# Kernel tuning notes

Measured on AMD Instinct MI355X. Metric: run time of the kernel, lower is better.

Reference implementation:

```python
import jax, jax.numpy as jnp
import numpy as np
from jax.scipy.special import erf

B, N, D = 4, 4096, 2
MU, ALPHA, BETA, SIGMA = 1.0, 0.8, 2.0, 0.02


def setup_inputs() -> dict:
    key = jax.random.key(0)
    k1, k2 = jax.random.split(key)
    locations = jax.random.uniform(k1, (B, N, D), dtype=jnp.float32)  # events in unit box
    times = jnp.sort(jax.random.uniform(k2, (B, N), dtype=jnp.float32), axis=-1)  # sorted event times
    # ragged sequence lengths via mask
    lengths = jnp.array([N, N - 256, N - 512, N - 1024], dtype=jnp.int32)
    mask = jnp.arange(N)[None, :] < lengths[:, None]
    return {
        "locations": locations,
        "times": times,
        "mask": mask,
        "mu": jnp.float32(MU),
        "alpha": jnp.float32(ALPHA),
        "beta": jnp.float32(BETA),
        "sigma": jnp.float32(SIGMA),
        "spatial_low": jnp.zeros((D,), jnp.float32),
        "spatial_high": jnp.ones((D,), jnp.float32),
        "t_end": jnp.float32(1.0),
    }


def reference(locations, times, mask, mu, alpha, beta, sigma, spatial_low, spatial_high, t_end):
    """Hawkes log_prob: sum_i log lambda*(s_i, t_i | H_{t_i}) - Lambda(D x [0, T])."""
    d = locations.shape[-1]
    # --- intensity at each event given its (strictly earlier, masked) history ---
    dt = times[:, :, None] - times[:, None, :]            # [B,N,N] t_i - t_j
    valid = (dt > 0.0) & mask[:, None, :]                 # causal + observed history
    dt_safe = jnp.where(valid, dt, 0.0)
    diff = locations[:, :, None, :] - locations[:, None, :, :]  # [B,N,N,D]
    sqdist = jnp.sum(diff * diff, axis=-1)                # [B,N,N]
    two_sig2 = 2.0 * sigma * sigma
    # fused exp of temporal decay * spatial Gaussian exponent
    kern = jnp.where(valid, jnp.exp(-beta * dt_safe - sqdist / two_sig2), 0.0)
    norm = beta / (jnp.pi * two_sig2) ** (d / 2)          # beta * (2*pi*sigma^2)^(-d/2)
    lam = mu + alpha * norm * jnp.sum(kern, axis=-1)      # [B,N]
    log_lam = jnp.sum(jnp.where(mask, jnp.log(lam), 0.0), axis=-1)  # [B]
    # --- compensator with erf boundary correction ---
    s_sqrt2 = sigma * jnp.sqrt(jnp.float32(2.0))
    cdf = 0.5 * (erf((spatial_high - locations) / s_sqrt2)
                 - erf((spatial_low - locations) / s_sqrt2))        # [B,N,D]
    in_domain_mass = jnp.prod(cdf, axis=-1)               # [B,N]
    temporal_mass = 1.0 - jnp.exp(-beta * (t_end - times))  # [B,N]
    area = jnp.prod(spatial_high - spatial_low)
    comp = mu * area * t_end + alpha * jnp.sum(
        jnp.where(mask, temporal_mass * in_domain_mass, 0.0), axis=-1)  # [B]
    return log_lam - comp
```

## Files before the change

### kernel.cpp

```cpp
#include <hip/hip_runtime.h>
#include <math.h>

#define NB 4096
#define BB 4
#define TI 256
#define TJ 256

#if __has_builtin(__builtin_amdgcn_exp2f)
#define EXP2F __builtin_amdgcn_exp2f
#else
#define EXP2F exp2f
#endif

__global__ __launch_bounds__(TI) void hawkes_pair(
    const float* __restrict__ loc, const float* __restrict__ times,
    const int* __restrict__ mask,
    const float* __restrict__ beta_p, const float* __restrict__ sigma_p,
    float* __restrict__ S)
{
    const int it = blockIdx.x;
    const int s  = blockIdx.y;
    if (s > it) return;
    const int b   = blockIdx.z;
    const int tid = threadIdx.x;

    const float beta  = beta_p[0];
    const float sigma = sigma_p[0];
    const float L2E = 1.4426950408889634f;
    const float nb  = -beta * L2E;
    const float nc  = -L2E / (2.0f * sigma * sigma);

    const int i = it * TI + tid;
    const float ti = times[b * NB + i];
    const float xi = loc[(b * NB + i) * 2 + 0];
    const float yi = loc[(b * NB + i) * 2 + 1];

    __shared__ float4 jt[TJ];
    {
        const int j = s * TJ + tid;
        const float tj = times[b * NB + j];
        const bool  mj = mask[b * NB + j] != 0;
        float4 v;
        v.x = mj ? tj : 2.0f;
        v.y = loc[(b * NB + j) * 2 + 0];
        v.z = loc[(b * NB + j) * 2 + 1];
        v.w = 0.0f;
        jt[tid] = v;
    }
    __syncthreads();

    float acc = 0.0f;
#pragma unroll 8
    for (int jj = 0; jj < TJ; ++jj) {
        float4 v = jt[jj];
        float dt = ti - v.x;
        float dx = xi - v.y;
        float dy = yi - v.z;
        float sq  = fmaf(dy, dy, dx * dx);
        float arg = fmaf(sq, nc, dt * nb);
        float e   = EXP2F(arg);
        acc += (dt > 0.0f) ? e : 0.0f;
    }
    atomicAdd(&S[b * NB + i], acc);
}

__global__ __launch_bounds__(256) void hawkes_finish(
    const float* __restrict__ loc, const float* __restrict__ times,
    const int* __restrict__ mask,
    const float* mu_p, const float* alpha_p, const float* beta_p, const float* sigma_p,
    const float* lo_p, const float* hi_p, const float* tend_p,
    const float* __restrict__ S, float* __restrict__ out)
{
    const int b   = blockIdx.x;
    const int tid = threadIdx.x;

    const float mu    = mu_p[0];
    const float alpha = alpha_p[0];
    const float beta  = beta_p[0];
    const float sigma = sigma_p[0];
    const float lo0 = lo_p[0], lo1 = lo_p[1];
    const float hi0 = hi_p[0], hi1 = hi_p[1];
    const float tend = tend_p[0];

    const float two_sig2 = 2.0f * sigma * sigma;
    const float norm = beta / ((float)M_PI * two_sig2);
    const float an = alpha * norm;
    const float inv_ss2 = 1.0f / (sigma * sqrtf(2.0f));

    float accL = 0.0f, accC = 0.0f;
    for (int i = tid; i < NB; i += 256) {
        if (mask[b * NB + i] != 0) {
            float lam = fmaf(an, S[b * NB + i], mu);
            accL += logf(lam);
            float tmass = 1.0f - expf(-beta * (tend - times[b * NB + i]));
            float x = loc[(b * NB + i) * 2 + 0];
            float y = loc[(b * NB + i) * 2 + 1];
            float cx = 0.5f * (erff((hi0 - x) * inv_ss2) - erff((lo0 - x) * inv_ss2));
            float cy = 0.5f * (erff((hi1 - y) * inv_ss2) - erff((lo1 - y) * inv_ss2));
            accC += tmass * cx * cy;
        }
    }

    __shared__ float redL[4], redC[4];
    for (int off = 32; off > 0; off >>= 1) {
        accL += __shfl_down(accL, off, 64);
        accC += __shfl_down(accC, off, 64);
    }
    const int wave = tid >> 6, lane = tid & 63;
    if (lane == 0) { redL[wave] = accL; redC[wave] = accC; }
    __syncthreads();
    if (tid == 0) {
        float L = redL[0] + redL[1] + redL[2] + redL[3];
        float C = redC[0] + redC[1] + redC[2] + redC[3];
        float area = (hi0 - lo0) * (hi1 - lo1);
        out[b] = L - (mu * area * tend + alpha * C);
    }
}

extern "C" void kernel_launch(void* const* d_in, const int* in_sizes, int n_in,
                              void* d_out, int out_size, void* d_ws, size_t ws_size,
                              hipStream_t stream) {
    const float* loc   = (const float*)d_in[0];
    const float* times = (const float*)d_in[1];
    const int*   mask  = (const int*)d_in[2];
    const float* mu_p    = (const float*)d_in[3];
    const float* alpha_p = (const float*)d_in[4];
    const float* beta_p  = (const float*)d_in[5];
    const float* sigma_p = (const float*)d_in[6];
    const float* lo_p    = (const float*)d_in[7];
    const float* hi_p    = (const float*)d_in[8];
    const float* tend_p  = (const float*)d_in[9];
    float* out = (float*)d_out;
    float* S   = (float*)d_ws;

    hipMemsetAsync(S, 0, BB * NB * sizeof(float), stream);

    dim3 grid(NB / TI, NB / TJ, BB);
    hawkes_pair<<<grid, TI, 0, stream>>>(loc, times, mask, beta_p, sigma_p, S);
    hawkes_finish<<<dim3(BB), 256, 0, stream>>>(loc, times, mask, mu_p, alpha_p, beta_p,
                                                sigma_p, lo_p, hi_p, tend_p, S, out);
}
```

Before: 106.0 us.

## Expand squared distance algebraically, two rows per thread, drop atomics and memset

The exponent is expanded as per-row and per-column precomputed terms plus a dot product, so each pair costs two FMAs, an add and an exp2. Each thread now handles two i rows that share the LDS j-tile, and tiles strictly below the diagonal skip the causal compare. Per-slice partial sums are written to a [B,NSL,N] workspace instead of using atomics, which removes the memset, and the finish kernel sums the slices using 1024 threads. The expanded form can lose precision through cancellation of large terms, and upper-triangle blocks still launch just to write zeros.

```diff
diff --git a/kernel.cpp b/kernel.cpp
--- a/kernel.cpp
+++ b/kernel.cpp
@@ -1,10 +1,13 @@
 #include <hip/hip_runtime.h>
 #include <math.h>
 
-#define NB 4096
-#define BB 4
-#define TI 256
-#define TJ 256
+#define NB  4096
+#define BB  4
+#define TI  512
+#define TJ  256
+#define NSL (NB / TJ)
+#define NIT (NB / TI)
+#define THR 256
 
 #if __has_builtin(__builtin_amdgcn_exp2f)
 #define EXP2F __builtin_amdgcn_exp2f
@@ -12,17 +15,26 @@
 #define EXP2F exp2f
 #endif
 
-__global__ __launch_bounds__(TI) void hawkes_pair(
+__global__ __launch_bounds__(THR) void hawkes_pair(
     const float* __restrict__ loc, const float* __restrict__ times,
     const int* __restrict__ mask,
     const float* __restrict__ beta_p, const float* __restrict__ sigma_p,
     float* __restrict__ S)
 {
-    const int it = blockIdx.x;
-    const int s  = blockIdx.y;
-    if (s > it) return;
+    const int it  = blockIdx.x;
+    const int s   = blockIdx.y;
     const int b   = blockIdx.z;
     const int tid = threadIdx.x;
+
+    const int i0 = it * TI + tid;
+    const int i1 = i0 + THR;
+    float* __restrict__ Srow = S + (size_t)(b * NSL + s) * NB;
+
+    if (s > 2 * it + 1) {
+        Srow[i0] = 0.0f;
+        Srow[i1] = 0.0f;
+        return;
+    }
 
     const float beta  = beta_p[0];
     const float sigma = sigma_p[0];
@@ -30,41 +42,58 @@
     const float nb  = -beta * L2E;
     const float nc  = -L2E / (2.0f * sigma * sigma);
 
-    const int i = it * TI + tid;
-    const float ti = times[b * NB + i];
-    const float xi = loc[(b * NB + i) * 2 + 0];
-    const float yi = loc[(b * NB + i) * 2 + 1];
+    const float t0 = times[b * NB + i0];
+    const float x0 = loc[(b * NB + i0) * 2 + 0];
+    const float y0 = loc[(b * NB + i0) * 2 + 1];
+    const float u0 = fmaf(nc, fmaf(x0, x0, y0 * y0), nb * t0);
+    const float t1 = times[b * NB + i1];
+    const float x1 = loc[(b * NB + i1) * 2 + 0];
+    const float y1 = loc[(b * NB + i1) * 2 + 1];
+    const float u1 = fmaf(nc, fmaf(x1, x1, y1 * y1), nb * t1);
 
     __shared__ float4 jt[TJ];
     {
-        const int j = s * TJ + tid;
+        const int j  = s * TJ + tid;
         const float tj = times[b * NB + j];
+        const float xj = loc[(b * NB + j) * 2 + 0];
+        const float yj = loc[(b * NB + j) * 2 + 1];
         const bool  mj = mask[b * NB + j] != 0;
         float4 v;
-        v.x = mj ? tj : 2.0f;
-        v.y = loc[(b * NB + j) * 2 + 0];
-        v.z = loc[(b * NB + j) * 2 + 1];
-        v.w = 0.0f;
+        v.x = mj ? fmaf(nc, fmaf(xj, xj, yj * yj), -nb * tj) : -3.0e38f;
+        v.y = mj ? (-2.0f * nc * xj) : 0.0f;
+        v.z = mj ? (-2.0f * nc * yj) : 0.0f;
+        v.w = mj ? tj : 2.0f;
         jt[tid] = v;
     }
     __syncthreads();
 
-    float acc = 0.0f;
+    float a0 = 0.0f, a1 = 0.0f;
+    if (s < 2 * it) {
 #pragma unroll 8
-    for (int jj = 0; jj < TJ; ++jj) {
-        float4 v = jt[jj];
-        float dt = ti - v.x;
-        float dx = xi - v.y;
-        float dy = yi - v.z;
-        float sq  = fmaf(dy, dy, dx * dx);
-        float arg = fmaf(sq, nc, dt * nb);
-        float e   = EXP2F(arg);
-        acc += (dt > 0.0f) ? e : 0.0f;
+        for (int jj = 0; jj < TJ; ++jj) {
+            float4 v = jt[jj];
+            float g0 = fmaf(v.y, x0, fmaf(v.z, y0, u0 + v.x));
+            float g1 = fmaf(v.y, x1, fmaf(v.z, y1, u1 + v.x));
+            a0 += EXP2F(g0);
+            a1 += EXP2F(g1);
+        }
+    } else {
+#pragma unroll 8
+        for (int jj = 0; jj < TJ; ++jj) {
+            float4 v = jt[jj];
+            float g0 = fmaf(v.y, x0, fmaf(v.z, y0, u0 + v.x));
+            float g1 = fmaf(v.y, x1, fmaf(v.z, y1, u1 + v.x));
+            float e0 = EXP2F(g0);
+            float e1 = EXP2F(g1);
+            a0 += (t0 > v.w) ? e0 : 0.0f;
+            a1 += (t1 > v.w) ? e1 : 0.0f;
+        }
     }
-    atomicAdd(&S[b * NB + i], acc);
+    Srow[i0] = a0;
+    Srow[i1] = a1;
 }
 
-__global__ __launch_bounds__(256) void hawkes_finish(
+__global__ __launch_bounds__(1024) void hawkes_finish(
     const float* __restrict__ loc, const float* __restrict__ times,
     const int* __restrict__ mask,
     const float* mu_p, const float* alpha_p, const float* beta_p, const float* sigma_p,
@@ -83,14 +112,17 @@
     const float tend = tend_p[0];
 
     const float two_sig2 = 2.0f * sigma * sigma;
-    const float norm = beta / ((float)M_PI * two_sig2);
-    const float an = alpha * norm;
+    const float an = alpha * beta / ((float)M_PI * two_sig2);
     const float inv_ss2 = 1.0f / (sigma * sqrtf(2.0f));
 
     float accL = 0.0f, accC = 0.0f;
-    for (int i = tid; i < NB; i += 256) {
+    for (int i = tid; i < NB; i += 1024) {
         if (mask[b * NB + i] != 0) {
-            float lam = fmaf(an, S[b * NB + i], mu);
+            float sum = 0.0f;
+#pragma unroll
+            for (int s = 0; s < NSL; ++s)
+                sum += S[(size_t)(b * NSL + s) * NB + i];
+            float lam = fmaf(an, sum, mu);
             accL += logf(lam);
             float tmass = 1.0f - expf(-beta * (tend - times[b * NB + i]));
             float x = loc[(b * NB + i) * 2 + 0];
@@ -101,7 +133,7 @@
         }
     }
 
-    __shared__ float redL[4], redC[4];
+    __shared__ float redL[16], redC[16];
     for (int off = 32; off > 0; off >>= 1) {
         accL += __shfl_down(accL, off, 64);
         accC += __shfl_down(accC, off, 64);
@@ -110,8 +142,9 @@
     if (lane == 0) { redL[wave] = accL; redC[wave] = accC; }
     __syncthreads();
     if (tid == 0) {
-        float L = redL[0] + redL[1] + redL[2] + redL[3];
-        float C = redC[0] + redC[1] + redC[2] + redC[3];
+        float L = 0.0f, C = 0.0f;
+#pragma unroll
+        for (int w = 0; w < 16; ++w) { L += redL[w]; C += redC[w]; }
         float area = (hi0 - lo0) * (hi1 - lo1);
         out[b] = L - (mu * area * tend + alpha * C);
     }
@@ -133,10 +166,8 @@
     float* out = (float*)d_out;
     float* S   = (float*)d_ws;
 
-    hipMemsetAsync(S, 0, BB * NB * sizeof(float), stream);
-
-    dim3 grid(NB / TI, NB / TJ, BB);
-    hawkes_pair<<<grid, TI, 0, stream>>>(loc, times, mask, beta_p, sigma_p, S);
-    hawkes_finish<<<dim3(BB), 256, 0, stream>>>(loc, times, mask, mu_p, alpha_p, beta_p,
-                                                sigma_p, lo_p, hi_p, tend_p, S, out);
+    dim3 grid(NIT, NSL, BB);
+    hawkes_pair<<<grid, THR, 0, stream>>>(loc, times, mask, beta_p, sigma_p, S);
+    hawkes_finish<<<dim3(BB), 1024, 0, stream>>>(loc, times, mask, mu_p, alpha_p, beta_p,
+                                                 sigma_p, lo_p, hi_p, tend_p, S, out);
 }
```

New measurement: 91.39 us. -13.8%, faster.
